# Kernel optimization log

Hardware: AMD Instinct MI355X
Metric: run time of the kernel (lower is better)

The kernel has to match this reference:

```python
import jax, jax.numpy as jnp
import numpy as np

B, INPUT_SIZE, HIDDEN, OUT, K = 16, 8192, 8, 34, 5
N = B * INPUT_SIZE            # 131072 nodes
E = N * 32                    # 4194304 edges


def setup_inputs() -> dict:
    key = jax.random.key(0)
    ks = jax.random.split(key, 8)
    x = jax.random.normal(ks[0], (N, 1), dtype=jnp.float32)
    edge_index = jax.random.randint(ks[1], (2, E), 0, N, dtype=jnp.int64)
    edge_attr = jax.random.normal(ks[2], (E,), dtype=jnp.float32)  # unused by forward, kept for signature fidelity
    batch = jnp.repeat(jnp.arange(B, dtype=jnp.int64), INPUT_SIZE)
    W1 = jax.random.normal(ks[3], (K, 1, HIDDEN), dtype=jnp.float32) * 0.3
    b1 = jnp.zeros((HIDDEN,), jnp.float32)
    W2 = jax.random.normal(ks[4], (K, HIDDEN, HIDDEN), dtype=jnp.float32) * 0.2
    b2 = jnp.zeros((HIDDEN,), jnp.float32)
    lin1_w = jax.random.normal(ks[5], (HIDDEN * INPUT_SIZE, 1000), dtype=jnp.float32) * 0.004
    lin1_b = jnp.zeros((1000,), jnp.float32)
    lin2_w = jax.random.normal(ks[6], (1000, OUT), dtype=jnp.float32) * 0.03
    lin2_b = jnp.zeros((OUT,), jnp.float32)
    return dict(x=x, edge_index=edge_index, edge_attr=edge_attr, batch=batch,
                W1=W1, b1=b1, W2=W2, b2=b2,
                lin1_w=lin1_w, lin1_b=lin1_b, lin2_w=lin2_w, lin2_b=lin2_b)


def _cheb_setup(edge_index, n, dtype):
    # PyG ChebConv with sym norm, lambda_max=2: Lhat = -D^{-1/2} A D^{-1/2},
    # diag 0 for deg>0 nodes, -1 for isolated nodes. Self loops removed.
    row, col = edge_index[0], edge_index[1]
    w = (row != col).astype(dtype)                      # remove self loops via zero weight
    deg = jax.ops.segment_sum(w, row, num_segments=n)
    dinv = jnp.where(deg > 0, jax.lax.rsqrt(jnp.maximum(deg, 1.0)), 0.0)
    norm = -dinv[row] * w * dinv[col]                   # [E]
    diag = jnp.where(deg > 0, 0.0, -1.0)[:, None]       # [N,1]
    return row, col, norm, diag


def _cheb_conv(x, W, b, row, col, norm, diag, n):
    # out = sum_k T_k(Lhat) x @ W[k] + b, Chebyshev recurrence over K slices
    def lhat(t):  # sparse matvec: scatter-add of weighted source features
        return jax.ops.segment_sum(norm[:, None] * t[row], col, num_segments=n) + diag * t
    Tx0 = x
    out = Tx0 @ W[0]
    Tx1 = lhat(Tx0)
    out = out + Tx1 @ W[1]
    for k in range(2, W.shape[0]):
        Tx2 = 2.0 * lhat(Tx1) - Tx0
        out = out + Tx2 @ W[k]
        Tx0, Tx1 = Tx1, Tx2
    return out + b


def reference(x, edge_index, edge_attr, batch, W1, b1, W2, b2, lin1_w, lin1_b, lin2_w, lin2_b):
    n = x.shape[0]
    row, col, norm, diag = _cheb_setup(edge_index, n, x.dtype)
    h = jax.nn.relu(_cheb_conv(x, W1, b1, row, col, norm, diag, n))
    h = jax.nn.relu(_cheb_conv(h, W2, b2, row, col, norm, diag, n))
    hidden = W2.shape[2]
    input_size = lin1_w.shape[0] // hidden
    bsz = n // input_size                                # == max(batch)+1
    h = h.reshape(bsz, input_size * hidden)
    h = jax.nn.relu(h @ lin1_w + lin1_b)
    return jnp.squeeze(h @ lin2_w + lin2_b)
```

## Files before the change

### kernel.cpp

```cpp
#include <hip/hip_runtime.h>

#define NN 131072
#define NE 4194304
#define HID 8
#define BSZ 16
#define MDIM 1000
#define ODIM 34
#define FC 128
#define NCHUNK 512
#define NB 256
#define EPB (NE / NB)
#define NBUK 1024
#define CNOD 128
#define NBUKR 512
#define SCAP 6144

typedef float f4v __attribute__((ext_vector_type(4)));
typedef float f2v __attribute__((ext_vector_type(2)));
typedef _Float16 h8v __attribute__((ext_vector_type(8)));
typedef _Float16 h2v __attribute__((ext_vector_type(2)));

__global__ __launch_bounds__(512) void bin_count(const int* __restrict__ ei,
                                                 int* __restrict__ colhist,
                                                 int* __restrict__ rowhist) {
    __shared__ int ch[NBUK];
    __shared__ int rh[NBUKR];
    int b = blockIdx.x, t = threadIdx.x;
    for (int i = t; i < NBUK; i += 512) ch[i] = 0;
    for (int i = t; i < NBUKR; i += 512) rh[i] = 0;
    __syncthreads();
    int base = b * EPB;
    for (int k = t; k < EPB; k += 512) {
        int e = base + k;
        int r = __builtin_nontemporal_load(&ei[e]);
        int c = __builtin_nontemporal_load(&ei[NE + e]);
        if (r != c) { atomicAdd(&ch[c >> 7], 1); atomicAdd(&rh[r >> 8], 1); }
    }
    __syncthreads();
    for (int i = t; i < NBUK; i += 512) colhist[b * NBUK + i] = ch[i];
    for (int i = t; i < NBUKR; i += 512) rowhist[b * NBUKR + i] = rh[i];
}

__global__ __launch_bounds__(NB) void bin_scan(int* __restrict__ hist,
                                               int* __restrict__ tot, int nbuckets) {
    __shared__ int s[NB];
    int i = blockIdx.x, t = threadIdx.x;
    int v = hist[t * nbuckets + i];
    s[t] = v; __syncthreads();
    for (int off = 1; off < NB; off <<= 1) {
        int x = (t >= off) ? s[t - off] : 0;
        __syncthreads(); s[t] += x; __syncthreads();
    }
    hist[t * nbuckets + i] = s[t] - v;
    if (t == NB - 1) tot[i] = s[t];
}

template <int M>
__global__ __launch_bounds__(256) void base_scan(const int* __restrict__ tot,
                                                 int* __restrict__ basev) {
    __shared__ int s[256];
    int t = threadIdx.x;
    int v[M]; int ps = 0;
    #pragma unroll
    for (int q = 0; q < M; ++q) { v[q] = tot[t * M + q]; ps += v[q]; }
    s[t] = ps; __syncthreads();
    for (int off = 1; off < 256; off <<= 1) {
        int x = (t >= off) ? s[t - off] : 0;
        __syncthreads(); s[t] += x; __syncthreads();
    }
    int run = s[t] - ps;
    #pragma unroll
    for (int q = 0; q < M; ++q) { basev[t * M + q] = run; run += v[q]; }
}

__global__ __launch_bounds__(512) void bin_fill(const int* __restrict__ ei,
                                                const int* __restrict__ colhist,
                                                const int* __restrict__ rowhist,
                                                const int* __restrict__ colbase,
                                                const int* __restrict__ rowbase,
                                                unsigned int* __restrict__ colbinned,
                                                unsigned char* __restrict__ rowbinned) {
    __shared__ int cc[NBUK];
    __shared__ int rc[NBUKR];
    int b = blockIdx.x, t = threadIdx.x;
    for (int i = t; i < NBUK; i += 512) cc[i] = colbase[i] + colhist[b * NBUK + i];
    for (int i = t; i < NBUKR; i += 512) rc[i] = rowbase[i] + rowhist[b * NBUKR + i];
    __syncthreads();
    int base = b * EPB;
    for (int k = t; k < EPB; k += 512) {
        int e = base + k;
        int r = __builtin_nontemporal_load(&ei[e]);
        int c = __builtin_nontemporal_load(&ei[NE + e]);
        if (r != c) {
            int p = atomicAdd(&cc[c >> 7], 1);
            colbinned[p] = ((unsigned)r << 7) | (unsigned)(c & 127);
            int q = atomicAdd(&rc[r >> 8], 1);
            rowbinned[q] = (unsigned char)(r & 255);
        }
    }
}

__global__ __launch_bounds__(256) void bucket_sort2(unsigned int* __restrict__ colbinned,
                                                    const int* __restrict__ colbase,
                                                    const int* __restrict__ coltot,
                                                    int* __restrict__ o,
                                                    int* __restrict__ sflag) {
    __shared__ unsigned int recs[SCAP];
    __shared__ int cnt[CNOD], scn[CNOD], cur[CNOD];
    int b = blockIdx.x, t = threadIdx.x;
    int s0 = colbase[b], n = coltot[b];
    if (n > SCAP) {
        if (t == 0) sflag[b] = 1;
        for (int i = t; i < CNOD; i += 256) o[b * CNOD + i] = s0;
        if (b == NBUK - 1 && t == 0) o[NN] = s0 + n;
        return;
    }
    if (t == 0) sflag[b] = 0;
    for (int i = t; i < CNOD; i += 256) cnt[i] = 0;
    __syncthreads();
    for (int i = t; i < n; i += 256) {
        unsigned int rec = colbinned[s0 + i];
        recs[i] = rec;
        atomicAdd(&cnt[rec & 127], 1);
    }
    __syncthreads();
    if (t < CNOD) scn[t] = cnt[t];
    __syncthreads();
    for (int off = 1; off < CNOD; off <<= 1) {
        int v = 0;
        if (t < CNOD && t >= off) v = scn[t - off];
        __syncthreads();
        if (t < CNOD) scn[t] += v;
        __syncthreads();
    }
    if (t < CNOD) {
        int ex = scn[t] - cnt[t];
        cur[t] = ex;
        o[b * CNOD + t] = s0 + ex;
    }
    __syncthreads();
    if (b == NBUK - 1 && t == 0) o[NN] = s0 + n;
    for (int i = t; i < n; i += 256) {
        unsigned int rec = recs[i];
        int p = atomicAdd(&cur[rec & 127], 1);
        colbinned[s0 + p] = rec;
    }
}

__global__ __launch_bounds__(256) void deg_finish(const unsigned char* __restrict__ rowbinned,
                                                  const int* __restrict__ rowbase,
                                                  const int* __restrict__ rowtot,
                                                  const float* __restrict__ x,
                                                  float* __restrict__ dinv,
                                                  float* __restrict__ rinv,
                                                  float* __restrict__ sx) {
    __shared__ int cnt[256];
    int b = blockIdx.x, t = threadIdx.x;
    cnt[t] = 0; __syncthreads();
    int s0 = rowbase[b], n = rowtot[b];
    for (int i = t; i < n; i += 256) atomicAdd(&cnt[rowbinned[s0 + i]], 1);
    __syncthreads();
    int d = cnt[t];
    int node = b * 256 + t;
    float dn = (d > 0) ? rsqrtf((float)d) : 0.f;
    dinv[node] = dn;
    rinv[node] = (d > 0) ? sqrtf((float)d) : 1.f;
    sx[node] = ((d > 0) ? dn : 1.f) * x[node];
}

template <int MODE>
__global__ __launch_bounds__(512) void cheb1_s(const unsigned int* __restrict__ colbinned,
                                               const int* __restrict__ colbase,
                                               const int* __restrict__ coltot,
                                               const int* __restrict__ o,
                                               const int* __restrict__ sflag,
                                               const float* __restrict__ dinv,
                                               const float* __restrict__ w_in,
                                               const float* __restrict__ wp2,
                                               float* __restrict__ w_out) {
    __shared__ float part[CNOD][4];
    __shared__ float accA[CNOD];
    int b = blockIdx.x, t = threadIdx.x;
    if (sflag[b]) {
        if (t < CNOD) accA[t] = 0.f;
        __syncthreads();
        int s0 = colbase[b], n = coltot[b];
        for (int i = t; i < n; i += 512) {
            unsigned int rec = colbinned[s0 + i];
            atomicAdd(&accA[rec & 127], w_in[rec >> 7]);
        }
        __syncthreads();
        if (t < CNOD) { part[t][0] = accA[t]; part[t][1] = 0.f; part[t][2] = 0.f; part[t][3] = 0.f; }
    } else {
        int nl = t >> 2, q = t & 3;
        int node = b * CNOD + nl;
        int os = o[node], len = o[node + 1] - os;
        int i0 = os + ((len * q) >> 2), i1 = os + ((len * (q + 1)) >> 2);
        float a = 0.f;
        for (int i = i0; i < i1; ++i) {
            unsigned int rec = __builtin_nontemporal_load(&colbinned[i]);
            a += w_in[rec >> 7];
        }
        part[nl][q] = a;
    }
    __syncthreads();
    if (t < CNOD) {
        float a = part[t][0] + part[t][1] + part[t][2] + part[t][3];
        int node = b * CNOD + t;
        float dn = dinv[node];
        float lh = (dn > 0.f) ? -dn * a : -w_in[node];
        float s = (dn > 0.f) ? dn : 1.f;
        w_out[node] = (MODE == 0) ? s * lh : s * (2.f * lh) - wp2[node];
    }
}

__global__ __launch_bounds__(256) void h1_kernel(const float* __restrict__ x,
        const float* __restrict__ wt1, const float* __restrict__ wt2,
        const float* __restrict__ wt3, const float* __restrict__ wt4,
        const float* __restrict__ dinv, const float* __restrict__ rinv,
        const float* __restrict__ W1, const float* __restrict__ b1,
        const float* __restrict__ W20, const float* __restrict__ b2,
        float* __restrict__ sh1, _Float16* __restrict__ s1t,
        float* __restrict__ accg) {
    int n = blockIdx.x * 256 + threadIdx.x;
    float rn = rinv[n], dn = dinv[n];
    float s = (dn > 0.f) ? dn : 1.f;
    float T0 = x[n], T1 = wt1[n] * rn, T2 = wt2[n] * rn, T3 = wt3[n] * rn, T4 = wt4[n] * rn;
    float h[HID];
    #pragma unroll
    for (int j = 0; j < HID; ++j) {
        float v = b1[j] + T0 * W1[j] + T1 * W1[8 + j] + T2 * W1[16 + j]
                + T3 * W1[24 + j] + T4 * W1[32 + j];
        h[j] = fmaxf(v, 0.f);
    }
    f4v sv0, sv1, av0, av1;
    h8v hv;
    #pragma unroll
    for (int j = 0; j < 4; ++j) { sv0[j] = s * h[j]; sv1[j] = s * h[4 + j]; }
    #pragma unroll
    for (int j = 0; j < 8; ++j) hv[j] = (_Float16)(s * h[j]);
    #pragma unroll
    for (int o2 = 0; o2 < HID; ++o2) {
        float v = b2[o2];
        #pragma unroll
        for (int j = 0; j < HID; ++j) v = fmaf(h[j], W20[j * 8 + o2], v);
        if (o2 < 4) av0[o2] = v; else av1[o2 - 4] = v;
    }
    *(f4v*)&sh1[n * 8] = sv0;  *(f4v*)&sh1[n * 8 + 4] = sv1;
    *(h8v*)&s1t[n * 8] = hv;
    *(f4v*)&accg[n * 8] = av0; *(f4v*)&accg[n * 8 + 4] = av1;
}

template <int MODE>
__global__ __launch_bounds__(512) void cheb8_s(const unsigned int* __restrict__ colbinned,
        const int* __restrict__ colbase, const int* __restrict__ coltot,
        const int* __restrict__ o, const int* __restrict__ sflag,
        const float* __restrict__ dinv, const float* __restrict__ rinv,
        const _Float16* __restrict__ w16_in, const float* __restrict__ w_in,
        const float* __restrict__ wp2,
        float* __restrict__ w_out, _Float16* __restrict__ w16_out,
        const float* __restrict__ Wk, float* __restrict__ accg) {
    __shared__ float vb[CNOD][HID];
    __shared__ float wk[64];
    __shared__ float accA[CNOD * 9];
    int b = blockIdx.x, t = threadIdx.x;
    if (t < 64) wk[t] = Wk[t];
    int nl = t >> 2, fp = t & 3;
    int node = b * CNOD + nl;
    int j0 = fp * 2;
    float a0, a1;
    if (!sflag[b]) {
        int os = o[node], oe = o[node + 1];
        a0 = 0.f; a1 = 0.f;
        int i = os;
        for (; i + 2 <= oe; i += 2) {
            unsigned int r0 = __builtin_nontemporal_load(&colbinned[i]);
            unsigned int r1 = __builtin_nontemporal_load(&colbinned[i + 1]);
            h2v v0 = *(const h2v*)&w16_in[(r0 >> 7) * 8 + j0];
            h2v v1 = *(const h2v*)&w16_in[(r1 >> 7) * 8 + j0];
            a0 += (float)v0[0] + (float)v1[0];
            a1 += (float)v0[1] + (float)v1[1];
        }
        if (i < oe) {
            unsigned int r0 = colbinned[i];
            h2v v0 = *(const h2v*)&w16_in[(r0 >> 7) * 8 + j0];
            a0 += (float)v0[0]; a1 += (float)v0[1];
        }
    } else {
        for (int i2 = t; i2 < CNOD * 9; i2 += 512) accA[i2] = 0.f;
        __syncthreads();
        int s0 = colbase[b], n = coltot[b];
        for (int i = t; i < n; i += 512) {
            unsigned int rec = colbinned[s0 + i];
            int r = rec >> 7, cl = rec & 127;
            h8v hv = *(const h8v*)&w16_in[r * 8];
            float* ap = &accA[cl * 9];
            atomicAdd(ap + 0, (float)hv[0]); atomicAdd(ap + 1, (float)hv[1]);
            atomicAdd(ap + 2, (float)hv[2]); atomicAdd(ap + 3, (float)hv[3]);
            atomicAdd(ap + 4, (float)hv[4]); atomicAdd(ap + 5, (float)hv[5]);
            atomicAdd(ap + 6, (float)hv[6]); atomicAdd(ap + 7, (float)hv[7]);
        }
        __syncthreads();
        a0 = accA[nl * 9 + j0];
        a1 = accA[nl * 9 + j0 + 1];
    }
    float dn = dinv[node];
    float lh0, lh1;
    if (dn > 0.f) { lh0 = -dn * a0; lh1 = -dn * a1; }
    else {
        f2v wp = *(const f2v*)&w_in[node * 8 + j0];
        lh0 = -wp[0]; lh1 = -wp[1];
    }
    float T0, T1;
    if (MODE == 0) {
        T0 = lh0; T1 = lh1;
        float sc = (dn > 0.f) ? dn : 1.f;
        f2v w; w[0] = sc * lh0; w[1] = sc * lh1;
        *(f2v*)&w_out[node * 8 + j0] = w;
        h2v wh; wh[0] = (_Float16)w[0]; wh[1] = (_Float16)w[1];
        *(h2v*)&w16_out[node * 8 + j0] = wh;
    } else if (MODE == 1) {
        float sc = (dn > 0.f) ? dn : 1.f;
        f2v p2 = *(const f2v*)&wp2[node * 8 + j0];
        f2v w; w[0] = sc * (2.f * lh0) - p2[0]; w[1] = sc * (2.f * lh1) - p2[1];
        *(f2v*)&w_out[node * 8 + j0] = w;
        h2v wh; wh[0] = (_Float16)w[0]; wh[1] = (_Float16)w[1];
        *(h2v*)&w16_out[node * 8 + j0] = wh;
        float rn = rinv[node];
        T0 = w[0] * rn; T1 = w[1] * rn;
    } else {
        f2v p2 = *(const f2v*)&wp2[node * 8 + j0];
        float rn = rinv[node];
        T0 = 2.f * lh0 - p2[0] * rn;
        T1 = 2.f * lh1 - p2[1] * rn;
    }
    vb[nl][j0] = T0; vb[nl][j0 + 1] = T1;
    __syncthreads();
    float s0 = 0.f, s1 = 0.f;
    #pragma unroll
    for (int q = 0; q < HID; ++q) {
        float vq = vb[nl][q];
        s0 = fmaf(vq, wk[q * 8 + j0], s0);
        s1 = fmaf(vq, wk[q * 8 + j0 + 1], s1);
    }
    f2v ag = *(const f2v*)&accg[node * 8 + j0];
    float r0 = ag[0] + s0, r1 = ag[1] + s1;
    f2v outv;
    outv[0] = (MODE == 2) ? fmaxf(r0, 0.f) : r0;
    outv[1] = (MODE == 2) ? fmaxf(r1, 0.f) : r1;
    *(f2v*)&accg[node * 8 + j0] = outv;
}

__global__ __launch_bounds__(256) void lin1_kernel(const float* __restrict__ h2,
                                                   const float* __restrict__ w,
                                                   float* __restrict__ part) {
    int chunk = blockIdx.x, t = threadIdx.x;
    int fbase = chunk * FC;
    __shared__ __align__(16) float a[FC * 20];
    for (int i = t; i < BSZ * FC; i += 256) {
        int bb = i >> 7, f = i & (FC - 1);
        a[f * 20 + bb] = h2[(size_t)bb * 65536 + fbase + f];
    }
    __syncthreads();
    f4v acc[16];
    #pragma unroll
    for (int bb = 0; bb < 16; ++bb) acc[bb] = (f4v)(0.f);
    int m = t * 4;
    if (m < MDIM) {
        for (int f = 0; f < FC; ++f) {
            f4v wv = __builtin_nontemporal_load((const f4v*)&w[(size_t)(fbase + f) * MDIM + m]);
            const f4v* ar = (const f4v*)&a[f * 20];
            f4v a0 = ar[0], a1 = ar[1], a2 = ar[2], a3 = ar[3];
            acc[0] += a0.x * wv;  acc[1] += a0.y * wv;  acc[2] += a0.z * wv;  acc[3] += a0.w * wv;
            acc[4] += a1.x * wv;  acc[5] += a1.y * wv;  acc[6] += a1.z * wv;  acc[7] += a1.w * wv;
            acc[8] += a2.x * wv;  acc[9] += a2.y * wv;  acc[10] += a2.z * wv; acc[11] += a2.w * wv;
            acc[12] += a3.x * wv; acc[13] += a3.y * wv; acc[14] += a3.z * wv; acc[15] += a3.w * wv;
        }
    }
    #pragma unroll
    for (int bb = 0; bb < 16; ++bb) {
        __builtin_nontemporal_store(acc[bb], (f4v*)&part[((size_t)chunk * 16 + bb) * 1024 + m]);
    }
}

__global__ __launch_bounds__(256) void hidden1(const float* __restrict__ part,
                                               float* __restrict__ part2) {
    int g = blockIdx.x >> 6;
    int off = (blockIdx.x & 63) * 256 + threadIdx.x;
    float s = 0.f;
    const float* p = part + (size_t)g * 64 * 16384 + off;
    for (int c = 0; c < 64; ++c) s += __builtin_nontemporal_load(&p[c * 16384]);
    part2[g * 16384 + off] = s;
}

__global__ __launch_bounds__(256) void hidden2(const float* __restrict__ part2,
                                               const float* __restrict__ lb,
                                               float* __restrict__ hid) {
    int off = blockIdx.x * 256 + threadIdx.x;
    int b = off >> 10, m = off & 1023;
    if (m >= MDIM) return;
    float s = lb[m];
    for (int g = 0; g < 8; ++g) s += part2[g * 16384 + off];
    hid[b * MDIM + m] = fmaxf(s, 0.f);
}

__global__ void out_kernel(const float* __restrict__ hid, const float* __restrict__ w2,
                           const float* __restrict__ b2, float* __restrict__ out) {
    int i = blockIdx.x * blockDim.x + threadIdx.x;
    if (i >= BSZ * ODIM) return;
    int b = i / ODIM, o = i % ODIM;
    float s = b2[o];
    for (int m = 0; m < MDIM; ++m) s = fmaf(hid[b * MDIM + m], w2[m * ODIM + o], s);
    out[i] = s;
}

extern "C" void kernel_launch(void* const* d_in, const int* in_sizes, int n_in,
                              void* d_out, int out_size, void* d_ws, size_t ws_size,
                              hipStream_t stream) {
    const float* x      = (const float*)d_in[0];
    const int*   ei     = (const int*)d_in[1];
    const float* W1     = (const float*)d_in[4];
    const float* b1     = (const float*)d_in[5];
    const float* W2     = (const float*)d_in[6];
    const float* b2     = (const float*)d_in[7];
    const float* lin1w  = (const float*)d_in[8];
    const float* lin1b  = (const float*)d_in[9];
    const float* lin2w  = (const float*)d_in[10];
    const float* lin2b  = (const float*)d_in[11];
    float* out = (float*)d_out;

    unsigned int* colbinned = (unsigned int*)d_ws;
    unsigned char* rowbinned = (unsigned char*)(colbinned + NE);
    _Float16* s1t = (_Float16*)rowbinned;
    _Float16* s2t = s1t + 8 * (size_t)NN;
    float* wA   = (float*)(rowbinned + NE);
    float* wB   = wA + 8 * (size_t)NN;
    float* sh1  = wB + 8 * (size_t)NN;
    float* wt1  = sh1 + 8 * (size_t)NN;
    float* wt2  = wt1 + NN;
    float* wt3  = wt2 + NN;
    float* wt4  = wt3 + NN;
    float* sx   = wt4 + NN;
    float* dinv = sx + NN;
    float* rinv = dinv + NN;
    int* colhist = (int*)(rinv + NN);
    int* rowhist = colhist + (size_t)NB * NBUK;
    int* coltot  = rowhist + (size_t)NB * NBUKR;
    int* colbase = coltot + NBUK;
    int* rowtot  = colbase + NBUK;
    int* rowbase = rowtot + NBUKR;
    int* o       = rowbase + NBUKR;
    int* sflag   = o + NN + 1;
    float* accg  = (float*)(sflag + NBUK);
    float* hid   = accg + 8 * (size_t)NN;
    float* part2 = hid + BSZ * 1024;
    float* part  = (float*)colbinned;

    bin_count<<<NB, 512, 0, stream>>>(ei, colhist, rowhist);
    bin_scan<<<NBUK, NB, 0, stream>>>(colhist, coltot, NBUK);
    bin_scan<<<NBUKR, NB, 0, stream>>>(rowhist, rowtot, NBUKR);
    base_scan<4><<<1, 256, 0, stream>>>(coltot, colbase);
    base_scan<2><<<1, 256, 0, stream>>>(rowtot, rowbase);
    bin_fill<<<NB, 512, 0, stream>>>(ei, colhist, rowhist, colbase, rowbase, colbinned, rowbinned);
    bucket_sort2<<<NBUK, 256, 0, stream>>>(colbinned, colbase, coltot, o, sflag);
    deg_finish<<<NBUKR, 256, 0, stream>>>(rowbinned, rowbase, rowtot, x, dinv, rinv, sx);

    cheb1_s<0><<<NBUK, 512, 0, stream>>>(colbinned, colbase, coltot, o, sflag, dinv, sx, nullptr, wt1);
    cheb1_s<1><<<NBUK, 512, 0, stream>>>(colbinned, colbase, coltot, o, sflag, dinv, wt1, sx, wt2);
    cheb1_s<1><<<NBUK, 512, 0, stream>>>(colbinned, colbase, coltot, o, sflag, dinv, wt2, wt1, wt3);
    cheb1_s<1><<<NBUK, 512, 0, stream>>>(colbinned, colbase, coltot, o, sflag, dinv, wt3, wt2, wt4);
    h1_kernel<<<NN / 256, 256, 0, stream>>>(x, wt1, wt2, wt3, wt4, dinv, rinv,
                                            W1, b1, W2, b2, sh1, s1t, accg);

    cheb8_s<0><<<NBUK, 512, 0, stream>>>(colbinned, colbase, coltot, o, sflag, dinv, rinv,
                                         s1t, sh1, nullptr, wA, s2t, W2 + 64, accg);
    cheb8_s<1><<<NBUK, 512, 0, stream>>>(colbinned, colbase, coltot, o, sflag, dinv, rinv,
                                         s2t, wA, sh1, wB, s1t, W2 + 128, accg);
    cheb8_s<1><<<NBUK, 512, 0, stream>>>(colbinned, colbase, coltot, o, sflag, dinv, rinv,
                                         s1t, wB, wA, wA, s2t, W2 + 192, accg);
    cheb8_s<2><<<NBUK, 512, 0, stream>>>(colbinned, colbase, coltot, o, sflag, dinv, rinv,
                                         s2t, wA, wB, nullptr, nullptr, W2 + 256, accg);

    lin1_kernel<<<NCHUNK, 256, 0, stream>>>(accg, lin1w, part);
    hidden1<<<512, 256, 0, stream>>>(part, part2);
    hidden2<<<64, 256, 0, stream>>>(part2, lin1b, hid);
    out_kernel<<<3, 256, 0, stream>>>(hid, lin2w, lin2b, out);
}
```

Measured before the change: 663.9 us.

## Gather full fp16 rows per edge in cheb8 and raise binning block count

```diff
diff --git a/kernel.cpp b/kernel.cpp
--- a/kernel.cpp
+++ b/kernel.cpp
@@ -8,7 +8,7 @@
 #define ODIM 34
 #define FC 128
 #define NCHUNK 512
-#define NB 256
+#define NB 1024
 #define EPB (NE / NB)
 #define NBUK 1024
 #define CNOD 128
@@ -18,7 +18,6 @@
 typedef float f4v __attribute__((ext_vector_type(4)));
 typedef float f2v __attribute__((ext_vector_type(2)));
 typedef _Float16 h8v __attribute__((ext_vector_type(8)));
-typedef _Float16 h2v __attribute__((ext_vector_type(2)));
 
 __global__ __launch_bounds__(512) void bin_count(const int* __restrict__ ei,
                                                  int* __restrict__ colhist,
@@ -45,13 +44,13 @@
                                                int* __restrict__ tot, int nbuckets) {
     __shared__ int s[NB];
     int i = blockIdx.x, t = threadIdx.x;
-    int v = hist[t * nbuckets + i];
+    int v = hist[(size_t)t * nbuckets + i];
     s[t] = v; __syncthreads();
     for (int off = 1; off < NB; off <<= 1) {
         int x = (t >= off) ? s[t - off] : 0;
         __syncthreads(); s[t] += x; __syncthreads();
     }
-    hist[t * nbuckets + i] = s[t] - v;
+    hist[(size_t)t * nbuckets + i] = s[t] - v;
     if (t == NB - 1) tot[i] = s[t];
 }
 
@@ -194,10 +193,9 @@
     } else {
         int nl = t >> 2, q = t & 3;
         int node = b * CNOD + nl;
-        int os = o[node], len = o[node + 1] - os;
-        int i0 = os + ((len * q) >> 2), i1 = os + ((len * (q + 1)) >> 2);
+        int os = o[node], oe = o[node + 1];
         float a = 0.f;
-        for (int i = i0; i < i1; ++i) {
+        for (int i = os + q; i < oe; i += 4) {
             unsigned int rec = __builtin_nontemporal_load(&colbinned[i]);
             a += w_in[rec >> 7];
         }
@@ -252,7 +250,7 @@
 }
 
 template <int MODE>
-__global__ __launch_bounds__(512) void cheb8_s(const unsigned int* __restrict__ colbinned,
+__global__ __launch_bounds__(512) void cheb8_e(const unsigned int* __restrict__ colbinned,
         const int* __restrict__ colbase, const int* __restrict__ coltot,
         const int* __restrict__ o, const int* __restrict__ sflag,
         const float* __restrict__ dinv, const float* __restrict__ rinv,
@@ -260,31 +258,24 @@
         const float* __restrict__ wp2,
         float* __restrict__ w_out, _Float16* __restrict__ w16_out,
         const float* __restrict__ Wk, float* __restrict__ accg) {
+    __shared__ float pl[CNOD][4][9];
     __shared__ float vb[CNOD][HID];
     __shared__ float wk[64];
     __shared__ float accA[CNOD * 9];
     int b = blockIdx.x, t = threadIdx.x;
     if (t < 64) wk[t] = Wk[t];
-    int nl = t >> 2, fp = t & 3;
+    int nl = t >> 2, l = t & 3;
     int node = b * CNOD + nl;
-    int j0 = fp * 2;
-    float a0, a1;
+    float a[8];
+    #pragma unroll
+    for (int j = 0; j < 8; ++j) a[j] = 0.f;
     if (!sflag[b]) {
         int os = o[node], oe = o[node + 1];
-        a0 = 0.f; a1 = 0.f;
-        int i = os;
-        for (; i + 2 <= oe; i += 2) {
-            unsigned int r0 = __builtin_nontemporal_load(&colbinned[i]);
-            unsigned int r1 = __builtin_nontemporal_load(&colbinned[i + 1]);
-            h2v v0 = *(const h2v*)&w16_in[(r0 >> 7) * 8 + j0];
-            h2v v1 = *(const h2v*)&w16_in[(r1 >> 7) * 8 + j0];
-            a0 += (float)v0[0] + (float)v1[0];
-            a1 += (float)v0[1] + (float)v1[1];
-        }
-        if (i < oe) {
-            unsigned int r0 = colbinned[i];
-            h2v v0 = *(const h2v*)&w16_in[(r0 >> 7) * 8 + j0];
-            a0 += (float)v0[0]; a1 += (float)v0[1];
+        for (int i = os + l; i < oe; i += 4) {
+            unsigned int rec = __builtin_nontemporal_load(&colbinned[i]);
+            h8v hv = *(const h8v*)&w16_in[(rec >> 7) * 8];
+            #pragma unroll
+            for (int j = 0; j < 8; ++j) a[j] += (float)hv[j];
         }
     } else {
         for (int i2 = t; i2 < CNOD * 9; i2 += 512) accA[i2] = 0.f;
@@ -295,60 +286,55 @@
             int r = rec >> 7, cl = rec & 127;
             h8v hv = *(const h8v*)&w16_in[r * 8];
             float* ap = &accA[cl * 9];
-            atomicAdd(ap + 0, (float)hv[0]); atomicAdd(ap + 1, (float)hv[1]);
-            atomicAdd(ap + 2, (float)hv[2]); atomicAdd(ap + 3, (float)hv[3]);
-            atomicAdd(ap + 4, (float)hv[4]); atomicAdd(ap + 5, (float)hv[5]);
-            atomicAdd(ap + 6, (float)hv[6]); atomicAdd(ap + 7, (float)hv[7]);
-        }
-        __syncthreads();
-        a0 = accA[nl * 9 + j0];
-        a1 = accA[nl * 9 + j0 + 1];
-    }
-    float dn = dinv[node];
-    float lh0, lh1;
-    if (dn > 0.f) { lh0 = -dn * a0; lh1 = -dn * a1; }
-    else {
-        f2v wp = *(const f2v*)&w_in[node * 8 + j0];
-        lh0 = -wp[0]; lh1 = -wp[1];
-    }
-    float T0, T1;
-    if (MODE == 0) {
-        T0 = lh0; T1 = lh1;
-        float sc = (dn > 0.f) ? dn : 1.f;
-        f2v w; w[0] = sc * lh0; w[1] = sc * lh1;
-        *(f2v*)&w_out[node * 8 + j0] = w;
-        h2v wh; wh[0] = (_Float16)w[0]; wh[1] = (_Float16)w[1];
-        *(h2v*)&w16_out[node * 8 + j0] = wh;
-    } else if (MODE == 1) {
-        float sc = (dn > 0.f) ? dn : 1.f;
-        f2v p2 = *(const f2v*)&wp2[node * 8 + j0];
-        f2v w; w[0] = sc * (2.f * lh0) - p2[0]; w[1] = sc * (2.f * lh1) - p2[1];
-        *(f2v*)&w_out[node * 8 + j0] = w;
-        h2v wh; wh[0] = (_Float16)w[0]; wh[1] = (_Float16)w[1];
-        *(h2v*)&w16_out[node * 8 + j0] = wh;
-        float rn = rinv[node];
-        T0 = w[0] * rn; T1 = w[1] * rn;
-    } else {
-        f2v p2 = *(const f2v*)&wp2[node * 8 + j0];
-        float rn = rinv[node];
-        T0 = 2.f * lh0 - p2[0] * rn;
-        T1 = 2.f * lh1 - p2[1] * rn;
-    }
-    vb[nl][j0] = T0; vb[nl][j0 + 1] = T1;
-    __syncthreads();
-    float s0 = 0.f, s1 = 0.f;
-    #pragma unroll
-    for (int q = 0; q < HID; ++q) {
-        float vq = vb[nl][q];
-        s0 = fmaf(vq, wk[q * 8 + j0], s0);
-        s1 = fmaf(vq, wk[q * 8 + j0 + 1], s1);
-    }
-    f2v ag = *(const f2v*)&accg[node * 8 + j0];
-    float r0 = ag[0] + s0, r1 = ag[1] + s1;
-    f2v outv;
-    outv[0] = (MODE == 2) ? fmaxf(r0, 0.f) : r0;
-    outv[1] = (MODE == 2) ? fmaxf(r1, 0.f) : r1;
-    *(f2v*)&accg[node * 8 + j0] = outv;
+            #pragma unroll
+            for (int j = 0; j < 8; ++j) atomicAdd(ap + j, (float)hv[j]);
+        }
+        __syncthreads();
+        if (l == 0) {
+            #pragma unroll
+            for (int j = 0; j < 8; ++j) a[j] = accA[nl * 9 + j];
+        }
+    }
+    #pragma unroll
+    for (int j = 0; j < 8; ++j) pl[nl][l][j] = a[j];
+    __syncthreads();
+    #pragma unroll
+    for (int k2 = 0; k2 < 2; ++k2) {
+        int idx = k2 * 512 + t;
+        int n2 = idx >> 3, jj = idx & 7;
+        int nd = b * CNOD + n2;
+        float asum = pl[n2][0][jj] + pl[n2][1][jj] + pl[n2][2][jj] + pl[n2][3][jj];
+        float dn = dinv[nd];
+        float lh = (dn > 0.f) ? -dn * asum : -w_in[nd * 8 + jj];
+        float T;
+        if (MODE == 0) {
+            T = lh;
+            float w = (dn > 0.f) ? dn * lh : lh;
+            w_out[nd * 8 + jj] = w;
+            w16_out[nd * 8 + jj] = (_Float16)w;
+        } else if (MODE == 1) {
+            float sc = (dn > 0.f) ? dn : 1.f;
+            float w = sc * (2.f * lh) - wp2[nd * 8 + jj];
+            w_out[nd * 8 + jj] = w;
+            w16_out[nd * 8 + jj] = (_Float16)w;
+            T = w * rinv[nd];
+        } else {
+            T = 2.f * lh - wp2[nd * 8 + jj] * rinv[nd];
+        }
+        vb[n2][jj] = T;
+    }
+    __syncthreads();
+    #pragma unroll
+    for (int k2 = 0; k2 < 2; ++k2) {
+        int idx = k2 * 512 + t;
+        int n2 = idx >> 3, jj = idx & 7;
+        int nd = b * CNOD + n2;
+        float sum = 0.f;
+        #pragma unroll
+        for (int q = 0; q < HID; ++q) sum = fmaf(vb[n2][q], wk[q * 8 + jj], sum);
+        float r2 = accg[nd * 8 + jj] + sum;
+        accg[nd * 8 + jj] = (MODE == 2) ? fmaxf(r2, 0.f) : r2;
+    }
 }
 
 __global__ __launch_bounds__(256) void lin1_kernel(const float* __restrict__ h2,
@@ -430,9 +416,9 @@
     float* out = (float*)d_out;
 
     unsigned int* colbinned = (unsigned int*)d_ws;
-    unsigned char* rowbinned = (unsigned char*)(colbinned + NE);
-    _Float16* s1t = (_Float16*)rowbinned;
+    _Float16* s1t = (_Float16*)(colbinned + NE);
     _Float16* s2t = s1t + 8 * (size_t)NN;
+    unsigned char* rowbinned = (unsigned char*)(s2t + 8 * (size_t)NN);
     float* wA   = (float*)(rowbinned + NE);
     float* wB   = wA + 8 * (size_t)NN;
     float* sh1  = wB + 8 * (size_t)NN;
@@ -454,7 +440,7 @@
     float* accg  = (float*)(sflag + NBUK);
     float* hid   = accg + 8 * (size_t)NN;
     float* part2 = hid + BSZ * 1024;
-    float* part  = (float*)colbinned;
+    float* part  = part2 + 8 * 16384;
 
     bin_count<<<NB, 512, 0, stream>>>(ei, colhist, rowhist);
     bin_scan<<<NBUK, NB, 0, stream>>>(colhist, coltot, NBUK);
@@ -472,13 +458,13 @@
     h1_kernel<<<NN / 256, 256, 0, stream>>>(x, wt1, wt2, wt3, wt4, dinv, rinv,
                                             W1, b1, W2, b2, sh1, s1t, accg);
 
-    cheb8_s<0><<<NBUK, 512, 0, stream>>>(colbinned, colbase, coltot, o, sflag, dinv, rinv,
+    cheb8_e<0><<<NBUK, 512, 0, stream>>>(colbinned, colbase, coltot, o, sflag, dinv, rinv,
                                          s1t, sh1, nullptr, wA, s2t, W2 + 64, accg);
-    cheb8_s<1><<<NBUK, 512, 0, stream>>>(colbinned, colbase, coltot, o, sflag, dinv, rinv,
+    cheb8_e<1><<<NBUK, 512, 0, stream>>>(colbinned, colbase, coltot, o, sflag, dinv, rinv,
                                          s2t, wA, sh1, wB, s1t, W2 + 128, accg);
-    cheb8_s<1><<<NBUK, 512, 0, stream>>>(colbinned, colbase, coltot, o, sflag, dinv, rinv,
+    cheb8_e<1><<<NBUK, 512, 0, stream>>>(colbinned, colbase, coltot, o, sflag, dinv, rinv,
                                          s1t, wB, wA, wA, s2t, W2 + 192, accg);
-    cheb8_s<2><<<NBUK, 512, 0, stream>>>(colbinned, colbase, coltot, o, sflag, dinv, rinv,
+    cheb8_e<2><<<NBUK, 512, 0, stream>>>(colbinned, colbase, coltot, o, sflag, dinv, rinv,
                                          s2t, wA, wB, nullptr, nullptr, W2 + 256, accg);
 
     lin1_kernel<<<NCHUNK, 256, 0, stream>>>(accg, lin1w, part);
```

Measured after the change: 624.1 us. -6.0%, faster.
